# Kernel optimization log

Measured on AMD Instinct MI355X. Metric: run time of the kernel, lower is better.

## Reference

```python
import jax, jax.numpy as jnp
import numpy as np

N = 100000
E = 300000
IN_C = 256
HID = 256   # 2 * out_channels
OUT_C = 128


def setup_inputs() -> dict:
    key = jax.random.key(0)
    k1, k2, k3, k4, k5 = jax.random.split(key, 5)
    x = jax.random.normal(k1, (N, IN_C), dtype=jnp.float32)
    edge_index = jax.random.randint(k2, (2, E), 0, N, dtype=jnp.int64)
    # Glorot-style init scale for GEMM weights
    W1 = jax.random.normal(k3, (IN_C, HID), dtype=jnp.float32) * (1.0 / np.sqrt(IN_C))
    b1 = jnp.zeros((HID,), dtype=jnp.float32)
    W2 = jax.random.normal(k4, (HID, OUT_C), dtype=jnp.float32) * (1.0 / np.sqrt(HID))
    b2 = jnp.zeros((OUT_C,), dtype=jnp.float32)
    return {"x": x, "edge_index": edge_index, "W1": W1, "b1": b1, "W2": W2, "b2": b2}


def _gcn_conv(x, W, b, src, dst, norm, n_nodes):
    # x: [N, Fin] -> transform then gather-scale-scatter aggregate
    h = x @ W                                   # [N, Fout]
    msgs = h[src] * norm[:, None]               # [E+N, Fout] (includes self-loops)
    out = jax.ops.segment_sum(msgs, dst, num_segments=n_nodes)
    return out + b


def _gcn_norm(edge_index, n_nodes):
    # add self-loops, compute symmetric deg^-1/2 normalization (PyG GCNConv default)
    loops = jnp.arange(n_nodes, dtype=edge_index.dtype)
    src = jnp.concatenate([edge_index[0], loops])
    dst = jnp.concatenate([edge_index[1], loops])
    deg = jax.ops.segment_sum(jnp.ones_like(dst, dtype=jnp.float32), dst, num_segments=n_nodes)
    dinv = jnp.where(deg > 0, jax.lax.rsqrt(deg), 0.0)
    norm = dinv[src] * dinv[dst]                # [E+N]
    return src, dst, norm


def reference(x, edge_index, W1, b1, W2, b2):
    n_nodes = x.shape[0]
    src, dst, norm = _gcn_norm(edge_index, n_nodes)
    h = _gcn_conv(x, W1, b1, src, dst, norm, n_nodes)
    h = jax.nn.relu(h)
    # dropout is identity in eval mode (reference baseline runs deterministic eval)
    return _gcn_conv(h, W2, b2, src, dst, norm, n_nodes)
```

## Files before the change

### kernel.cpp

```cpp
#include <hip/hip_runtime.h>
#include <stdint.h>

#define IN_C  256
#define HID   256
#define OUT_C 128
#define SCAN_BS 1024

typedef __bf16 bf16x8 __attribute__((ext_vector_type(8)));
typedef float  f32x4  __attribute__((ext_vector_type(4)));
typedef unsigned short u16x8 __attribute__((ext_vector_type(8)));
typedef unsigned short u16x4 __attribute__((ext_vector_type(4)));
typedef unsigned short u16x2 __attribute__((ext_vector_type(2)));
typedef unsigned int u32;

static __device__ __forceinline__ unsigned short f2b(float f) {
    union { float f; uint32_t u; } v; v.f = f;
    uint32_t r = v.u + 0x7fffu + ((v.u >> 16) & 1u);
    return (unsigned short)(r >> 16);
}
static __device__ __forceinline__ float b2f(unsigned short b) {
    union { uint32_t u; float f; } v; v.u = ((uint32_t)b) << 16;
    return v.f;
}
static __device__ __forceinline__ u32 cvtpk(float lo, float hi) {
    u32 r;
    asm("v_cvt_pk_bf16_f32 %0, %1, %2" : "=v"(r) : "v"(lo), "v"(hi));
    return r;
}

typedef __attribute__((address_space(1))) const u32 gas_u32;
typedef __attribute__((address_space(3))) u32 las_u32;
static __device__ __forceinline__ void gld16(const void* g, void* l) {
    __builtin_amdgcn_global_load_lds((gas_u32*)g, (las_u32*)l, 16, 0, 0);
}
#define SB() __builtin_amdgcn_sched_barrier(0)

__global__ void k_init(const float* __restrict__ W1, const float* __restrict__ W2,
                       unsigned short* __restrict__ W1G, unsigned short* __restrict__ W2T,
                       int* __restrict__ cnt, int n) {
    int i = blockIdx.x * blockDim.x + threadIdx.x;
    if (i < 65536) {
        int gi = i >> 3, j = i & 7;
        int kt = gi >> 10, c = (gi >> 8) & 3, nn = gi & 255;
        W1G[i] = f2b(W1[(size_t)(kt * 32 + c * 8 + j) * HID + nn]);
    }
    if (i < 32768) W2T[i] = f2b(W2[(i & 255) * OUT_C + (i >> 8)]);
    if (i < n) cnt[i] = 0;
}

__global__ void k_count(const int* __restrict__ dst, int* __restrict__ cnt, int e) {
    int i = blockIdx.x * blockDim.x + threadIdx.x;
    if (i < e) atomicAdd(&cnt[dst[i]], 1);
}

__global__ __launch_bounds__(SCAN_BS) void k_scan_block(
    const int* __restrict__ cnt, int* __restrict__ rs, int* __restrict__ bsum, int n) {
    __shared__ int s[SCAN_BS];
    const int tid = threadIdx.x;
    const int i = blockIdx.x * SCAN_BS + tid;
    int v = (i < n) ? cnt[i] + 1 : 0;
    s[tid] = v;
    __syncthreads();
    for (int off = 1; off < SCAN_BS; off <<= 1) {
        int t = (tid >= off) ? s[tid - off] : 0;
        __syncthreads();
        s[tid] += t;
        __syncthreads();
    }
    if (i < n) rs[i] = s[tid] - v;
    if (tid == SCAN_BS - 1) bsum[blockIdx.x] = s[tid];
}

__global__ void k_scan_sums(int* __restrict__ bsum, int nb) {
    __shared__ int s[128];
    const int tid = threadIdx.x;
    int v = (tid < nb) ? bsum[tid] : 0;
    s[tid] = v;
    __syncthreads();
    for (int off = 1; off < 128; off <<= 1) {
        int t = (tid >= off) ? s[tid - off] : 0;
        __syncthreads();
        s[tid] += t;
        __syncthreads();
    }
    if (tid < nb) bsum[tid] = s[tid] - v;
}

__global__ void k_scan_add(int* __restrict__ rs, int* __restrict__ cur,
                           const int* __restrict__ bsum, const int* __restrict__ cnt,
                           float* __restrict__ dinv, int2* __restrict__ csrw, int n) {
    int i = blockIdx.x * blockDim.x + threadIdx.x;
    if (i < n) {
        int v = rs[i] + bsum[i >> 10];
        rs[i] = v;
        cur[i] = v + 1;
        float dp1 = (float)(cnt[i] + 1);
        dinv[i] = rsqrtf(dp1);
        csrw[v] = make_int2(i, __float_as_int(1.0f / dp1));
    }
}

__global__ void k_fill(const int* __restrict__ src, const int* __restrict__ dst,
                       const float* __restrict__ dinv,
                       int* __restrict__ cur, int2* __restrict__ csrw, int e) {
    int i = blockIdx.x * blockDim.x + threadIdx.x;
    if (i < e) {
        int s = src[i], d = dst[i];
        int p = atomicAdd(&cur[d], 1);
        csrw[p] = make_int2(s, __float_as_int(dinv[s] * dinv[d]));
    }
}

__global__ __launch_bounds__(512) void k_gemm1(
    const float* __restrict__ x, const unsigned short* __restrict__ W1G,
    unsigned short* __restrict__ t1, int n) {
    __shared__ __align__(16) unsigned short As[2][4096];
    __shared__ __align__(16) unsigned short Bs[3][8192];
    const int tid  = threadIdx.x;
    const int row0 = blockIdx.x * 128;
    const int wid = tid >> 6, lane = tid & 63;
    const int wm = wid >> 2, wn = wid & 3;
    const int lrow = lane & 15, lgrp = lane >> 4;

    const int ar = tid & 127, ac = tid >> 7;
    int arow = row0 + ar; if (arow > n - 1) arow = n - 1;
    const float* aptr = x + (size_t)arow * IN_C + ac * 8;

    f32x4 acc[4][4];
    #pragma unroll
    for (int i = 0; i < 4; ++i)
        #pragma unroll
        for (int j = 0; j < 4; ++j)
            acc[i][j] = (f32x4){0.f, 0.f, 0.f, 0.f};

    {
        f32x4 a = *(const f32x4*)aptr;
        f32x4 b = *(const f32x4*)(aptr + 4);
        SB();
        #pragma unroll
        for (int i = 0; i < 2; ++i) {
            int chunk = tid + 512 * i;
            gld16(&W1G[(size_t)chunk * 8], &Bs[0][chunk * 8]);
        }
        #pragma unroll
        for (int i = 0; i < 2; ++i) {
            int chunk = tid + 512 * i;
            gld16(&W1G[(size_t)8192 + chunk * 8], &Bs[1][chunk * 8]);
        }
        SB();
        union { u32 w[4]; u16x8 v; } pk;
        pk.w[0] = cvtpk(a[0], a[1]); pk.w[1] = cvtpk(a[2], a[3]);
        pk.w[2] = cvtpk(b[0], b[1]); pk.w[3] = cvtpk(b[2], b[3]);
        *(u16x8*)&As[0][ac * 1024 + ar * 8] = pk.v;
        asm volatile("s_waitcnt vmcnt(2) lgkmcnt(0)" ::: "memory");
        SB();
        __builtin_amdgcn_s_barrier();
        SB();
    }

    #pragma unroll
    for (int t = 0; t < 8; ++t) {
        const int cb = t % 3;
        const int ca = t & 1;
        f32x4 pa, pb;
        if (t < 7) {
            const float* ap = aptr + (t + 1) * 32;
            pa = *(const f32x4*)ap;
            pb = *(const f32x4*)(ap + 4);
        }
        SB();
        if (t < 6) {
            const int nb3 = (t + 2) % 3;
            #pragma unroll
            for (int i = 0; i < 2; ++i) {
                int chunk = tid + 512 * i;
                gld16(&W1G[(size_t)(t + 2) * 8192 + chunk * 8], &Bs[nb3][chunk * 8]);
            }
        }
        SB();
        bf16x8 av[4], bv[4];
        #pragma unroll
        for (int mf = 0; mf < 4; ++mf) {
            int r = wm * 64 + mf * 16 + lrow;
            av[mf] = *(const bf16x8*)&As[ca][lgrp * 1024 + r * 8];
        }
        #pragma unroll
        for (int nf = 0; nf < 4; ++nf) {
            int cc = wn * 64 + nf * 16 + lrow;
            bv[nf] = *(const bf16x8*)&Bs[cb][lgrp * 2048 + cc * 8];
        }
        #pragma unroll
        for (int mf = 0; mf < 4; ++mf)
            #pragma unroll
            for (int nf = 0; nf < 4; ++nf)
                acc[mf][nf] = __builtin_amdgcn_mfma_f32_16x16x32_bf16(
                    av[mf], bv[nf], acc[mf][nf], 0, 0, 0);
        SB();
        if (t < 7) {
            union { u32 w[4]; u16x8 v; } pk;
            pk.w[0] = cvtpk(pa[0], pa[1]); pk.w[1] = cvtpk(pa[2], pa[3]);
            pk.w[2] = cvtpk(pb[0], pb[1]); pk.w[3] = cvtpk(pb[2], pb[3]);
            *(u16x8*)&As[(t + 1) & 1][ac * 1024 + ar * 8] = pk.v;
            if (t < 6)
                asm volatile("s_waitcnt vmcnt(2) lgkmcnt(0)" ::: "memory");
            else
                asm volatile("s_waitcnt vmcnt(0) lgkmcnt(0)" ::: "memory");
            SB();
            __builtin_amdgcn_s_barrier();
            SB();
        }
    }

    __syncthreads();
    unsigned short* Cs = &Bs[0][0];
    #pragma unroll
    for (int mf = 0; mf < 4; ++mf) {
        #pragma unroll
        for (int nf = 0; nf < 4; ++nf)
            #pragma unroll
            for (int j = 0; j < 4; ++j)
                Cs[(wm * 16 + lgrp * 4 + j) * 260 + wn * 64 + nf * 16 + lrow] =
                    f2b(acc[mf][nf][j]);
        __syncthreads();
        #pragma unroll
        for (int it = 0; it < 2; ++it) {
            int chunk = tid + 512 * it;
            int lr = chunk >> 5, c8 = chunk & 31;
            u16x8 v = *(const u16x8*)&Cs[lr * 260 + c8 * 8];
            int grow = row0 + (lr >> 4) * 64 + mf * 16 + (lr & 15);
            if (grow < n)
                *(u16x8*)&t1[(size_t)grow * HID + c8 * 8] = v;
        }
        if (mf < 3) __syncthreads();
    }
}

__global__ __launch_bounds__(256) void k_agg1(
    const unsigned short* __restrict__ t1, const int* __restrict__ rs,
    const int* __restrict__ cnt, const int2* __restrict__ csrw,
    const float* __restrict__ b1, unsigned short* __restrict__ out1, int n) {
    const int w = blockIdx.x * 4 + (threadIdx.x >> 6);
    const int n0 = w * 4;
    if (n0 >= n) return;
    const int lane = threadIdx.x & 63;
    const int ch = lane * 4;
    int beg[4], m[4];
    #pragma unroll
    for (int q = 0; q < 4; ++q) {
        int node = n0 + q;
        bool valid = node < n;
        beg[q] = valid ? rs[node] : 0;
        m[q]   = valid ? cnt[node] + 1 : 0;
    }
    float acc[4][4];
    #pragma unroll
    for (int q = 0; q < 4; ++q)
        #pragma unroll
        for (int k = 0; k < 4; ++k) acc[q][k] = 0.f;
    const int m01 = m[0] > m[1] ? m[0] : m[1];
    const int m23 = m[2] > m[3] ? m[2] : m[3];
    const int mmax = m01 > m23 ? m01 : m23;

    int2 p0[4], p1[4];
    u16x4 r0[4];
    #pragma unroll
    for (int q = 0; q < 4; ++q) p0[q] = csrw[beg[q]];
    #pragma unroll
    for (int q = 0; q < 4; ++q) {
        int idx = (1 < m[q]) ? beg[q] + 1 : beg[q];
        p1[q] = csrw[idx];
    }
    #pragma unroll
    for (int q = 0; q < 4; ++q)
        r0[q] = *(const u16x4*)&t1[(size_t)p0[q].x * HID + ch];

    for (int j = 0; j < mmax; ++j) {
        int2 p2[4];
        u16x4 r1[4];
        #pragma unroll
        for (int q = 0; q < 4; ++q) {
            int jn = j + 2;
            int idx = (jn < m[q]) ? beg[q] + jn : beg[q];
            p2[q] = csrw[idx];
        }
        #pragma unroll
        for (int q = 0; q < 4; ++q)
            r1[q] = *(const u16x4*)&t1[(size_t)p1[q].x * HID + ch];
        #pragma unroll
        for (int q = 0; q < 4; ++q) {
            if (j < m[q]) {
                float wq = __int_as_float(p0[q].y);
                acc[q][0] += b2f(r0[q][0]) * wq; acc[q][1] += b2f(r0[q][1]) * wq;
                acc[q][2] += b2f(r0[q][2]) * wq; acc[q][3] += b2f(r0[q][3]) * wq;
            }
            p0[q] = p1[q]; p1[q] = p2[q]; r0[q] = r1[q];
        }
    }
    float4 bb = *(const float4*)(b1 + ch);
    #pragma unroll
    for (int q = 0; q < 4; ++q) {
        int node = n0 + q;
        if (node < n) {
            u16x4 o;
            o[0] = f2b(fmaxf(acc[q][0] + bb.x, 0.f));
            o[1] = f2b(fmaxf(acc[q][1] + bb.y, 0.f));
            o[2] = f2b(fmaxf(acc[q][2] + bb.z, 0.f));
            o[3] = f2b(fmaxf(acc[q][3] + bb.w, 0.f));
            *(u16x4*)&out1[(size_t)node * HID + ch] = o;
        }
    }
}

__global__ __launch_bounds__(256) void k_gemm2(
    const unsigned short* __restrict__ out1, const unsigned short* __restrict__ W2T,
    unsigned short* __restrict__ t2, int n) {
    __shared__ __align__(16) unsigned short As[128 * 64];
    __shared__ __align__(16) unsigned short Bs[128 * 64];
    const int tid  = threadIdx.x;
    const int row0 = blockIdx.x * 128;
    const int wid = tid >> 6, lane = tid & 63;
    const int wm = wid >> 1, wn = wid & 1;
    const int lrow = lane & 15, lgrp = lane >> 4;

    f32x4 acc[4][4];
    #pragma unroll
    for (int i = 0; i < 4; ++i)
        #pragma unroll
        for (int j = 0; j < 4; ++j)
            acc[i][j] = (f32x4){0.f, 0.f, 0.f, 0.f};

    for (int kt = 0; kt < 4; ++kt) {
        #pragma unroll
        for (int i = 0; i < 4; ++i) {
            int chunk = tid + 256 * i;
            int r = chunk >> 3, c = chunk & 7;
            int grow = row0 + r; if (grow > n - 1) grow = n - 1;
            gld16(&out1[(size_t)grow * HID + kt * 64 + ((c ^ (r & 7)) * 8)],
                  &As[chunk * 8]);
        }
        #pragma unroll
        for (int i = 0; i < 4; ++i) {
            int chunk = tid + 256 * i;
            int nn = chunk >> 3, c = chunk & 7;
            gld16(&W2T[(size_t)nn * 256 + kt * 64 + ((c ^ (nn & 7)) * 8)],
                  &Bs[chunk * 8]);
        }
        __syncthreads();
        #pragma unroll
        for (int kk = 0; kk < 2; ++kk) {
            const int cfrag = kk * 4 + lgrp;
            bf16x8 av[4], bv[4];
            #pragma unroll
            for (int mf = 0; mf < 4; ++mf) {
                int r = wm * 64 + mf * 16 + lrow;
                av[mf] = *(const bf16x8*)&As[r * 64 + ((cfrag ^ (r & 7)) * 8)];
            }
            #pragma unroll
            for (int nf = 0; nf < 4; ++nf) {
                int cc = wn * 64 + nf * 16 + lrow;
                bv[nf] = *(const bf16x8*)&Bs[cc * 64 + ((cfrag ^ (cc & 7)) * 8)];
            }
            #pragma unroll
            for (int mf = 0; mf < 4; ++mf)
                #pragma unroll
                for (int nf = 0; nf < 4; ++nf)
                    acc[mf][nf] = __builtin_amdgcn_mfma_f32_16x16x32_bf16(
                        av[mf], bv[nf], acc[mf][nf], 0, 0, 0);
        }
        __syncthreads();
    }

    unsigned short* Cs = &Bs[0];
    #pragma unroll
    for (int mf = 0; mf < 4; ++mf) {
        #pragma unroll
        for (int nf = 0; nf < 4; ++nf)
            #pragma unroll
            for (int j = 0; j < 4; ++j)
                Cs[(wm * 16 + lgrp * 4 + j) * 132 + wn * 64 + nf * 16 + lrow] =
                    f2b(acc[mf][nf][j]);
        __syncthreads();
        #pragma unroll
        for (int it = 0; it < 2; ++it) {
            int chunk = tid + 256 * it;
            int lr = chunk >> 4, c8 = chunk & 15;
            u16x8 v = *(const u16x8*)&Cs[lr * 132 + c8 * 8];
            int grow = row0 + (lr >> 4) * 64 + mf * 16 + (lr & 15);
            if (grow < n)
                *(u16x8*)&t2[(size_t)grow * OUT_C + c8 * 8] = v;
        }
        if (mf < 3) __syncthreads();
    }
}

__global__ __launch_bounds__(256) void k_agg2(
    const unsigned short* __restrict__ t2, const int* __restrict__ rs,
    const int* __restrict__ cnt, const int2* __restrict__ csrw,
    const float* __restrict__ b2, float* __restrict__ out, int n) {
    const int w = blockIdx.x * 4 + (threadIdx.x >> 6);
    const int n0 = w * 4;
    if (n0 >= n) return;
    const int lane = threadIdx.x & 63;
    const int ch = lane * 2;
    int beg[4], m[4];
    #pragma unroll
    for (int q = 0; q < 4; ++q) {
        int node = n0 + q;
        bool valid = node < n;
        beg[q] = valid ? rs[node] : 0;
        m[q]   = valid ? cnt[node] + 1 : 0;
    }
    float acc[4][2];
    #pragma unroll
    for (int q = 0; q < 4; ++q) { acc[q][0] = 0.f; acc[q][1] = 0.f; }
    const int m01 = m[0] > m[1] ? m[0] : m[1];
    const int m23 = m[2] > m[3] ? m[2] : m[3];
    const int mmax = m01 > m23 ? m01 : m23;

    int2 p0[4], p1[4];
    u16x2 r0[4];
    #pragma unroll
    for (int q = 0; q < 4; ++q) p0[q] = csrw[beg[q]];
    #pragma unroll
    for (int q = 0; q < 4; ++q) {
        int idx = (1 < m[q]) ? beg[q] + 1 : beg[q];
        p1[q] = csrw[idx];
    }
    #pragma unroll
    for (int q = 0; q < 4; ++q)
        r0[q] = *(const u16x2*)&t2[(size_t)p0[q].x * OUT_C + ch];

    for (int j = 0; j < mmax; ++j) {
        int2 p2[4];
        u16x2 r1[4];
        #pragma unroll
        for (int q = 0; q < 4; ++q) {
            int jn = j + 2;
            int idx = (jn < m[q]) ? beg[q] + jn : beg[q];
            p2[q] = csrw[idx];
        }
        #pragma unroll
        for (int q = 0; q < 4; ++q)
            r1[q] = *(const u16x2*)&t2[(size_t)p1[q].x * OUT_C + ch];
        #pragma unroll
        for (int q = 0; q < 4; ++q) {
            if (j < m[q]) {
                float wq = __int_as_float(p0[q].y);
                acc[q][0] += b2f(r0[q][0]) * wq; acc[q][1] += b2f(r0[q][1]) * wq;
            }
            p0[q] = p1[q]; p1[q] = p2[q]; r0[q] = r1[q];
        }
    }
    float2 bb = *(const float2*)(b2 + ch);
    #pragma unroll
    for (int q = 0; q < 4; ++q) {
        int node = n0 + q;
        if (node < n)
            *(float2*)&out[(size_t)node * OUT_C + ch] =
                make_float2(acc[q][0] + bb.x, acc[q][1] + bb.y);
    }
}

extern "C" void kernel_launch(void* const* d_in, const int* in_sizes, int n_in,
                              void* d_out, int out_size, void* d_ws, size_t ws_size,
                              hipStream_t stream) {
    const float* x  = (const float*)d_in[0];
    const int*   ei = (const int*)d_in[1];
    const float* W1 = (const float*)d_in[2];
    const float* b1 = (const float*)d_in[3];
    const float* W2 = (const float*)d_in[4];
    const float* b2 = (const float*)d_in[5];
    float* out = (float*)d_out;

    const int n = in_sizes[0] / IN_C;
    const int e = in_sizes[1] / 2;
    const int* src = ei;
    const int* dst = ei + e;

    int*   cnt  = (int*)d_ws;
    int*   rs   = cnt + n;
    int*   cur  = rs + n;
    int*   bsum = cur + n;
    float* dinv = (float*)(bsum + 128);
    int2*  csrw = (int2*)(dinv + n);
    unsigned short* W1G = (unsigned short*)(csrw + (size_t)e + n);
    unsigned short* W2T = W1G + 65536;
    unsigned short* t1  = W2T + 32768;
    unsigned short* out1 = t1 + (size_t)n * HID;
    unsigned short* t2  = t1;

    const int nb = (n + SCAN_BS - 1) / SCAN_BS;

    k_init<<<(n + 255) / 256, 256, 0, stream>>>(W1, W2, W1G, W2T, cnt, n);
    k_count<<<(e + 255) / 256, 256, 0, stream>>>(dst, cnt, e);
    k_scan_block<<<nb, SCAN_BS, 0, stream>>>(cnt, rs, bsum, n);
    k_scan_sums<<<1, 128, 0, stream>>>(bsum, nb);
    k_scan_add<<<(n + 255) / 256, 256, 0, stream>>>(rs, cur, bsum, cnt, dinv, csrw, n);
    k_fill<<<(e + 255) / 256, 256, 0, stream>>>(src, dst, dinv, cur, csrw, e);

    const int mb = (n + 127) / 128;
    k_gemm1<<<mb, 512, 0, stream>>>(x, W1G, t1, n);
    const int aggblk = (n + 15) / 16;
    k_agg1<<<aggblk, 256, 0, stream>>>(t1, rs, cnt, csrw, b1, out1, n);
    k_gemm2<<<mb, 256, 0, stream>>>(out1, W2T, t2, n);
    k_agg2<<<aggblk, 256, 0, stream>>>(t2, rs, cnt, csrw, b2, out, n);
}
```

Before: 192.3 us.

## Fuse block-sum scan into scan_add and double GEMM1 row tile to 256

```diff
diff --git a/kernel.cpp b/kernel.cpp
--- a/kernel.cpp
+++ b/kernel.cpp
@@ -71,27 +71,25 @@
     if (tid == SCAN_BS - 1) bsum[blockIdx.x] = s[tid];
 }
 
-__global__ void k_scan_sums(int* __restrict__ bsum, int nb) {
-    __shared__ int s[128];
-    const int tid = threadIdx.x;
-    int v = (tid < nb) ? bsum[tid] : 0;
-    s[tid] = v;
-    __syncthreads();
-    for (int off = 1; off < 128; off <<= 1) {
-        int t = (tid >= off) ? s[tid - off] : 0;
-        __syncthreads();
-        s[tid] += t;
-        __syncthreads();
-    }
-    if (tid < nb) bsum[tid] = s[tid] - v;
-}
-
 __global__ void k_scan_add(int* __restrict__ rs, int* __restrict__ cur,
                            const int* __restrict__ bsum, const int* __restrict__ cnt,
                            float* __restrict__ dinv, int2* __restrict__ csrw, int n) {
-    int i = blockIdx.x * blockDim.x + threadIdx.x;
+    __shared__ int red[256];
+    const int tid = threadIdx.x;
+    const int K = (int)(blockIdx.x >> 2);
+    int s = 0;
+    for (int j = tid; j < K; j += 256) s += bsum[j];
+    red[tid] = s;
+    __syncthreads();
+    #pragma unroll
+    for (int off = 128; off > 0; off >>= 1) {
+        if (tid < off) red[tid] += red[tid + off];
+        __syncthreads();
+    }
+    const int base = red[0];
+    int i = blockIdx.x * 256 + tid;
     if (i < n) {
-        int v = rs[i] + bsum[i >> 10];
+        int v = rs[i] + base;
         rs[i] = v;
         cur[i] = v + 1;
         float dp1 = (float)(cnt[i] + 1);
@@ -111,18 +109,18 @@
     }
 }
 
-__global__ __launch_bounds__(512) void k_gemm1(
+__global__ __launch_bounds__(1024, 8) void k_gemm1(
     const float* __restrict__ x, const unsigned short* __restrict__ W1G,
     unsigned short* __restrict__ t1, int n) {
-    __shared__ __align__(16) unsigned short As[2][4096];
+    __shared__ __align__(16) unsigned short As[2][8192];
     __shared__ __align__(16) unsigned short Bs[3][8192];
     const int tid  = threadIdx.x;
-    const int row0 = blockIdx.x * 128;
+    const int row0 = blockIdx.x * 256;
     const int wid = tid >> 6, lane = tid & 63;
     const int wm = wid >> 2, wn = wid & 3;
     const int lrow = lane & 15, lgrp = lane >> 4;
 
-    const int ar = tid & 127, ac = tid >> 7;
+    const int ar = tid & 255, ac = tid >> 8;
     int arow = row0 + ar; if (arow > n - 1) arow = n - 1;
     const float* aptr = x + (size_t)arow * IN_C + ac * 8;
 
@@ -137,22 +135,14 @@
         f32x4 a = *(const f32x4*)aptr;
         f32x4 b = *(const f32x4*)(aptr + 4);
         SB();
-        #pragma unroll
-        for (int i = 0; i < 2; ++i) {
-            int chunk = tid + 512 * i;
-            gld16(&W1G[(size_t)chunk * 8], &Bs[0][chunk * 8]);
-        }
-        #pragma unroll
-        for (int i = 0; i < 2; ++i) {
-            int chunk = tid + 512 * i;
-            gld16(&W1G[(size_t)8192 + chunk * 8], &Bs[1][chunk * 8]);
-        }
+        gld16(&W1G[(size_t)tid * 8], &Bs[0][tid * 8]);
+        gld16(&W1G[(size_t)8192 + tid * 8], &Bs[1][tid * 8]);
         SB();
         union { u32 w[4]; u16x8 v; } pk;
         pk.w[0] = cvtpk(a[0], a[1]); pk.w[1] = cvtpk(a[2], a[3]);
         pk.w[2] = cvtpk(b[0], b[1]); pk.w[3] = cvtpk(b[2], b[3]);
-        *(u16x8*)&As[0][ac * 1024 + ar * 8] = pk.v;
-        asm volatile("s_waitcnt vmcnt(2) lgkmcnt(0)" ::: "memory");
+        *(u16x8*)&As[0][ac * 2048 + ar * 8] = pk.v;
+        asm volatile("s_waitcnt vmcnt(1) lgkmcnt(0)" ::: "memory");
         SB();
         __builtin_amdgcn_s_barrier();
         SB();
@@ -169,20 +159,14 @@
             pb = *(const f32x4*)(ap + 4);
         }
         SB();
-        if (t < 6) {
-            const int nb3 = (t + 2) % 3;
-            #pragma unroll
-            for (int i = 0; i < 2; ++i) {
-                int chunk = tid + 512 * i;
-                gld16(&W1G[(size_t)(t + 2) * 8192 + chunk * 8], &Bs[nb3][chunk * 8]);
-            }
-        }
+        if (t < 6)
+            gld16(&W1G[(size_t)(t + 2) * 8192 + tid * 8], &Bs[(t + 2) % 3][tid * 8]);
         SB();
         bf16x8 av[4], bv[4];
         #pragma unroll
         for (int mf = 0; mf < 4; ++mf) {
             int r = wm * 64 + mf * 16 + lrow;
-            av[mf] = *(const bf16x8*)&As[ca][lgrp * 1024 + r * 8];
+            av[mf] = *(const bf16x8*)&As[ca][lgrp * 2048 + r * 8];
         }
         #pragma unroll
         for (int nf = 0; nf < 4; ++nf) {
@@ -200,9 +184,9 @@
             union { u32 w[4]; u16x8 v; } pk;
             pk.w[0] = cvtpk(pa[0], pa[1]); pk.w[1] = cvtpk(pa[2], pa[3]);
             pk.w[2] = cvtpk(pb[0], pb[1]); pk.w[3] = cvtpk(pb[2], pb[3]);
-            *(u16x8*)&As[(t + 1) & 1][ac * 1024 + ar * 8] = pk.v;
+            *(u16x8*)&As[(t + 1) & 1][ac * 2048 + ar * 8] = pk.v;
             if (t < 6)
-                asm volatile("s_waitcnt vmcnt(2) lgkmcnt(0)" ::: "memory");
+                asm volatile("s_waitcnt vmcnt(1) lgkmcnt(0)" ::: "memory");
             else
                 asm volatile("s_waitcnt vmcnt(0) lgkmcnt(0)" ::: "memory");
             SB();
@@ -224,7 +208,7 @@
         __syncthreads();
         #pragma unroll
         for (int it = 0; it < 2; ++it) {
-            int chunk = tid + 512 * it;
+            int chunk = tid + 1024 * it;
             int lr = chunk >> 5, c8 = chunk & 31;
             u16x8 v = *(const u16x8*)&Cs[lr * 260 + c8 * 8];
             int grow = row0 + (lr >> 4) * 64 + mf * 16 + (lr & 15);
@@ -494,14 +478,14 @@
     k_init<<<(n + 255) / 256, 256, 0, stream>>>(W1, W2, W1G, W2T, cnt, n);
     k_count<<<(e + 255) / 256, 256, 0, stream>>>(dst, cnt, e);
     k_scan_block<<<nb, SCAN_BS, 0, stream>>>(cnt, rs, bsum, n);
-    k_scan_sums<<<1, 128, 0, stream>>>(bsum, nb);
     k_scan_add<<<(n + 255) / 256, 256, 0, stream>>>(rs, cur, bsum, cnt, dinv, csrw, n);
     k_fill<<<(e + 255) / 256, 256, 0, stream>>>(src, dst, dinv, cur, csrw, e);
 
-    const int mb = (n + 127) / 128;
-    k_gemm1<<<mb, 512, 0, stream>>>(x, W1G, t1, n);
+    const int mb1 = (n + 255) / 256;
+    k_gemm1<<<mb1, 1024, 0, stream>>>(x, W1G, t1, n);
     const int aggblk = (n + 15) / 16;
     k_agg1<<<aggblk, 256, 0, stream>>>(t1, rs, cnt, csrw, b1, out1, n);
-    k_gemm2<<<mb, 256, 0, stream>>>(out1, W2T, t2, n);
+    const int mb2 = (n + 127) / 128;
+    k_gemm2<<<mb2, 256, 0, stream>>>(out1, W2T, t2, n);
     k_agg2<<<aggblk, 256, 0, stream>>>(t2, rs, cnt, csrw, b2, out, n);
 }
```

Result: slower. 400.2 us (+108.1%).
